# Kernel optimization log

Measured on AMD Instinct MI355X. Metric: run time of the kernel, lower is better.

The kernel has to match this reference:

```python
import jax, jax.numpy as jnp
import numpy as np


def setup_inputs() -> dict:
    key = jax.random.key(0)
    k1, k2, k3 = jax.random.split(key, 3)
    B, C, K, W, H = 8, 512, 512, 64, 64
    x = jax.random.normal(k1, (B, C, W, H), dtype=jnp.float32)
    y = jax.random.normal(k2, (B, K, W, H), dtype=jnp.float32)
    scale = jax.random.uniform(k3, (1,), dtype=jnp.float32)
    return {"x": x, "y": y, "scale": scale}


def reference(x, y, scale):
    B, C, W, H = x.shape
    K = y.shape[1]
    xq = x.reshape(B, C, W * H)            # [B, C, N]
    yk = y.reshape(B, K, W * H)            # [B, K, N]
    # energy = Q @ K^T : [B, C, K]
    energy = jnp.einsum('bcn,bkn->bck', xq, yk)
    # inverted max-subtract softmax over last dim (K)
    energy_new = jnp.max(energy, axis=-1, keepdims=True) - energy
    attention = jax.nn.softmax(energy_new, axis=-1)  # [B, C, K]
    # out = attention @ V : [B, C, N]
    out = jnp.einsum('bck,bkn->bcn', attention, yk).reshape(B, C, W, H)
    return x + scale * out
```

## Files before the change

kernel.cpp:

```cpp
#include <hip/hip_runtime.h>
#include <hip/hip_bf16.h>
#include <stdint.h>

#define BB 8
#define CC 512
#define KK 512
#define NN 4096

typedef __bf16 bf16x8 __attribute__((ext_vector_type(8)));
typedef float f32x4 __attribute__((ext_vector_type(4)));
typedef __attribute__((address_space(3))) uint8_t* lds_ptr_t;
typedef const __attribute__((address_space(1))) uint8_t* gbl_ptr_t;

static __device__ __forceinline__ unsigned short bf16_bits(float f) {
    __bf16 h = (__bf16)f;
    return __builtin_bit_cast(unsigned short, h);
}

__global__ void __launch_bounds__(256) split_hi_lo(const float* __restrict__ in,
        unsigned short* __restrict__ hi, unsigned short* __restrict__ lo, int n4) {
    int idx = blockIdx.x * blockDim.x + threadIdx.x;
    int stride = gridDim.x * blockDim.x;
    const float4* in4 = (const float4*)in;
    ushort4* h4 = (ushort4*)hi;
    ushort4* l4 = (ushort4*)lo;
    for (int i = idx; i < n4; i += stride) {
        float4 v = in4[i];
        float a[4] = {v.x, v.y, v.z, v.w};
        unsigned short hb[4], lb[4];
        #pragma unroll
        for (int j = 0; j < 4; ++j) {
            __bf16 h = (__bf16)a[j];
            float hf = (float)h;
            __bf16 l = (__bf16)(a[j] - hf);
            hb[j] = __builtin_bit_cast(unsigned short, h);
            lb[j] = __builtin_bit_cast(unsigned short, l);
        }
        h4[i] = make_ushort4(hb[0], hb[1], hb[2], hb[3]);
        l4[i] = make_ushort4(lb[0], lb[1], lb[2], lb[3]);
    }
}

__global__ void __launch_bounds__(256) energy_gemm(
        const unsigned short* __restrict__ xh, const unsigned short* __restrict__ xl,
        const unsigned short* __restrict__ yh, const unsigned short* __restrict__ yl,
        float* __restrict__ epart) {
    __shared__ __align__(16) uint8_t smem[4 * 16384];
    const int ktile = blockIdx.x;
    const int ctile = blockIdx.y;
    const int b = blockIdx.z >> 2;
    const int quarter = blockIdx.z & 3;
    const int t = threadIdx.x;
    const int wave = t >> 6, lane = t & 63;

    const size_t rowB = (size_t)NN * 2;
    const uint8_t* srcBase[4];
    srcBase[0] = (const uint8_t*)xh + ((size_t)b * CC + ctile * 128) * rowB + (size_t)quarter * 2048;
    srcBase[1] = (const uint8_t*)xl + ((size_t)b * CC + ctile * 128) * rowB + (size_t)quarter * 2048;
    srcBase[2] = (const uint8_t*)yh + ((size_t)b * KK + ktile * 128) * rowB + (size_t)quarter * 2048;
    srcBase[3] = (const uint8_t*)yl + ((size_t)b * KK + ktile * 128) * rowB + (size_t)quarter * 2048;

    f32x4 acc[4][4] = {};
    const int waveRow = wave >> 1, waveCol = wave & 1;

    for (int step = 0; step < 16; ++step) {
        const size_t colByte = (size_t)step * 128;
        #pragma unroll
        for (int i = 0; i < 16; ++i) {
            const int tile = i >> 2;
            const int lc = (i & 3) * 4 + wave;
            const int u = lc * 64 + lane;
            const int r = u >> 3;
            const int c3 = (u & 7) ^ (r & 7);
            const uint8_t* src = srcBase[tile] + (size_t)r * rowB + colByte + c3 * 16;
            __builtin_amdgcn_global_load_lds((gbl_ptr_t)src,
                (lds_ptr_t)(smem + tile * 16384 + lc * 1024), 16, 0, 0);
        }
        __syncthreads();
        #pragma unroll
        for (int kf = 0; kf < 2; ++kf) {
            bf16x8 fah[4], fal[4], fbh[4], fbl[4];
            #pragma unroll
            for (int m = 0; m < 4; ++m) {
                int r = waveRow * 64 + m * 16 + (lane & 15);
                int c3 = (kf * 4 + (lane >> 4)) ^ (r & 7);
                fah[m] = *(const bf16x8*)(smem + 0 * 16384 + r * 128 + c3 * 16);
                fal[m] = *(const bf16x8*)(smem + 1 * 16384 + r * 128 + c3 * 16);
            }
            #pragma unroll
            for (int n = 0; n < 4; ++n) {
                int r = waveCol * 64 + n * 16 + (lane & 15);
                int c3 = (kf * 4 + (lane >> 4)) ^ (r & 7);
                fbh[n] = *(const bf16x8*)(smem + 2 * 16384 + r * 128 + c3 * 16);
                fbl[n] = *(const bf16x8*)(smem + 3 * 16384 + r * 128 + c3 * 16);
            }
            #pragma unroll
            for (int m = 0; m < 4; ++m)
            #pragma unroll
            for (int n = 0; n < 4; ++n) {
                acc[m][n] = __builtin_amdgcn_mfma_f32_16x16x32_bf16(fah[m], fbh[n], acc[m][n], 0, 0, 0);
                acc[m][n] = __builtin_amdgcn_mfma_f32_16x16x32_bf16(fah[m], fbl[n], acc[m][n], 0, 0, 0);
                acc[m][n] = __builtin_amdgcn_mfma_f32_16x16x32_bf16(fal[m], fbh[n], acc[m][n], 0, 0, 0);
            }
        }
        __syncthreads();
    }

    float* eout = epart + (size_t)quarter * BB * CC * KK + (size_t)b * CC * KK;
    const int row0 = ctile * 128 + waveRow * 64;
    const int col0 = ktile * 128 + waveCol * 64;
    #pragma unroll
    for (int m = 0; m < 4; ++m)
    #pragma unroll
    for (int n = 0; n < 4; ++n)
    #pragma unroll
    for (int j = 0; j < 4; ++j) {
        int rr = row0 + m * 16 + (lane >> 4) * 4 + j;
        int cc2 = col0 + n * 16 + (lane & 15);
        eout[(size_t)rr * KK + cc2] = acc[m][n][j];
    }
}

__global__ void __launch_bounds__(256) softmax_inv(
        const float* __restrict__ e, unsigned short* __restrict__ att) {
    const int t = threadIdx.x;
    const int wave = t >> 6, lane = t & 63;
    const int row = blockIdx.x * 4 + wave;
    const size_t Q = (size_t)BB * CC * KK;
    const float* p0 = e + (size_t)row * KK;
    float v[8];
    float mn = 3.0e38f;
    #pragma unroll
    for (int i = 0; i < 8; ++i) {
        int c = lane + i * 64;
        v[i] = p0[c] + p0[Q + c] + p0[2 * Q + c] + p0[3 * Q + c];
        mn = fminf(mn, v[i]);
    }
    #pragma unroll
    for (int off = 32; off > 0; off >>= 1) mn = fminf(mn, __shfl_xor(mn, off));
    float p[8]; float s = 0.f;
    #pragma unroll
    for (int i = 0; i < 8; ++i) { p[i] = __expf(mn - v[i]); s += p[i]; }
    #pragma unroll
    for (int off = 32; off > 0; off >>= 1) s += __shfl_xor(s, off);
    float inv = 1.0f / s;
    unsigned short* arow = att + (size_t)row * KK;
    #pragma unroll
    for (int i = 0; i < 8; ++i) arow[lane + i * 64] = bf16_bits(p[i] * inv);
}

__global__ void __launch_bounds__(256) transpose_bf16(
        const unsigned short* __restrict__ yh, unsigned short* __restrict__ yT) {
    __shared__ unsigned short tile[64][66];
    const int n0 = blockIdx.x * 64, k0 = blockIdx.y * 64, b = blockIdx.z;
    const int t = threadIdx.x;
    const unsigned short* src = yh + (size_t)b * KK * NN;
    unsigned short* dst = yT + (size_t)b * NN * KK;
    #pragma unroll
    for (int i = 0; i < 2; ++i) {
        int idx = t + 256 * i;
        int r = idx >> 3;
        int c8 = (idx & 7) * 8;
        uint4 v = *(const uint4*)(src + (size_t)(k0 + r) * NN + n0 + c8);
        unsigned int w[4] = {v.x, v.y, v.z, v.w};
        #pragma unroll
        for (int q = 0; q < 4; ++q) {
            tile[r][c8 + 2 * q]     = (unsigned short)(w[q] & 0xffffu);
            tile[r][c8 + 2 * q + 1] = (unsigned short)(w[q] >> 16);
        }
    }
    __syncthreads();
    #pragma unroll
    for (int i = 0; i < 16; ++i) {
        int idx = t + 256 * i;
        int rn = idx >> 6;
        int ck = idx & 63;
        dst[(size_t)(n0 + rn) * KK + k0 + ck] = tile[ck][rn];
    }
}

__global__ void __launch_bounds__(256) pv_residual(
        const unsigned short* __restrict__ att, const unsigned short* __restrict__ yT,
        const float* __restrict__ x, const float* __restrict__ scale,
        float* __restrict__ out) {
    __shared__ __align__(16) uint8_t smem[2 * 16384];
    const int ntile = blockIdx.x;
    const int ctile = blockIdx.y;
    const int b = blockIdx.z;
    const int t = threadIdx.x;
    const int wave = t >> 6, lane = t & 63;
    const size_t rowB = (size_t)KK * 2;
    const uint8_t* srcA = (const uint8_t*)att + ((size_t)b * CC + ctile * 128) * rowB;
    const uint8_t* srcB = (const uint8_t*)yT  + ((size_t)b * NN + ntile * 128) * rowB;

    f32x4 acc[4][4] = {};
    const int waveRow = wave >> 1, waveCol = wave & 1;

    for (int step = 0; step < 8; ++step) {
        const size_t colByte = (size_t)step * 128;
        #pragma unroll
        for (int i = 0; i < 8; ++i) {
            const uint8_t* base = (i < 4) ? srcA : srcB;
            const int tile = i >> 2;
            const int lc = (i & 3) * 4 + wave;
            const int u = lc * 64 + lane;
            const int r = u >> 3;
            const int c3 = (u & 7) ^ (r & 7);
            const uint8_t* src = base + (size_t)r * rowB + colByte + c3 * 16;
            __builtin_amdgcn_global_load_lds((gbl_ptr_t)src,
                (lds_ptr_t)(smem + tile * 16384 + lc * 1024), 16, 0, 0);
        }
        __syncthreads();
        #pragma unroll
        for (int kf = 0; kf < 2; ++kf) {
            bf16x8 fa[4], fb[4];
            #pragma unroll
            for (int m = 0; m < 4; ++m) {
                int r = waveRow * 64 + m * 16 + (lane & 15);
                int c3 = (kf * 4 + (lane >> 4)) ^ (r & 7);
                fa[m] = *(const bf16x8*)(smem + r * 128 + c3 * 16);
            }
            #pragma unroll
            for (int n = 0; n < 4; ++n) {
                int r = waveCol * 64 + n * 16 + (lane & 15);
                int c3 = (kf * 4 + (lane >> 4)) ^ (r & 7);
                fb[n] = *(const bf16x8*)(smem + 16384 + r * 128 + c3 * 16);
            }
            #pragma unroll
            for (int m = 0; m < 4; ++m)
            #pragma unroll
            for (int n = 0; n < 4; ++n)
                acc[m][n] = __builtin_amdgcn_mfma_f32_16x16x32_bf16(fa[m], fb[n], acc[m][n], 0, 0, 0);
        }
        __syncthreads();
    }

    const float s = scale[0];
    const int row0 = ctile * 128 + waveRow * 64;
    const int col0 = ntile * 128 + waveCol * 64;
    #pragma unroll
    for (int m = 0; m < 4; ++m)
    #pragma unroll
    for (int n = 0; n < 4; ++n)
    #pragma unroll
    for (int j = 0; j < 4; ++j) {
        int rr = row0 + m * 16 + (lane >> 4) * 4 + j;
        int cc2 = col0 + n * 16 + (lane & 15);
        size_t idx = ((size_t)b * CC + rr) * NN + cc2;
        out[idx] = x[idx] + s * acc[m][n][j];
    }
}

extern "C" void kernel_launch(void* const* d_in, const int* in_sizes, int n_in,
                              void* d_out, int out_size, void* d_ws, size_t ws_size,
                              hipStream_t stream) {
    const float* x = (const float*)d_in[0];
    const float* y = (const float*)d_in[1];
    const float* scale = (const float*)d_in[2];
    float* out = (float*)d_out;
    uint8_t* ws = (uint8_t*)d_ws;
    const size_t MB = 1024 * 1024;
    unsigned short* xh = (unsigned short*)(ws + 0 * MB);
    unsigned short* xl = (unsigned short*)(ws + 32 * MB);
    unsigned short* yh = (unsigned short*)(ws + 64 * MB);
    unsigned short* yl = (unsigned short*)(ws + 96 * MB);
    float* epart = out;
    unsigned short* yT  = (unsigned short*)(ws + 0 * MB);
    unsigned short* att = (unsigned short*)(ws + 32 * MB);

    const int n4 = BB * CC * NN / 4;
    split_hi_lo<<<4096, 256, 0, stream>>>(x, xh, xl, n4);
    split_hi_lo<<<4096, 256, 0, stream>>>(y, yh, yl, n4);
    energy_gemm<<<dim3(4, 4, BB * 4), 256, 0, stream>>>(xh, xl, yh, yl, epart);
    transpose_bf16<<<dim3(NN / 64, KK / 64, BB), 256, 0, stream>>>(yh, yT);
    softmax_inv<<<dim3(BB * CC / 4), 256, 0, stream>>>(epart, att);
    pv_residual<<<dim3(NN / 128, CC / 128, BB), 256, 0, stream>>>(att, yT, x, scale, out);
}
```

Baseline: 302.3 us.

## Fuse y split with transpose and remap GEMM blocks for XCD locality

Replaces the separate y hi/lo split and bf16 transpose kernels with one kernel. It splits y into hi/lo and writes the transposed hi copy from an LDS tile, so the extra pass that re-reads yh and one launch go away. The energy and PV GEMMs move to a 1D grid with index remapping, so blocks sharing a batch or slice land on the same XCD and can share its L2. Workspace buffers are rearranged, with xl and the energy partials now placed in the output buffer.

```diff
diff --git a/kernel.cpp b/kernel.cpp
--- a/kernel.cpp
+++ b/kernel.cpp
@@ -41,15 +41,61 @@
     }
 }
 
+__global__ void __launch_bounds__(256) split_y_T(const float* __restrict__ y,
+        unsigned short* __restrict__ yh, unsigned short* __restrict__ yl,
+        unsigned short* __restrict__ yT) {
+    __shared__ unsigned short tile[64][66];
+    const int n0 = blockIdx.x * 64, k0 = blockIdx.y * 64, b = blockIdx.z;
+    const int t = threadIdx.x;
+    const float* src = y + (size_t)b * KK * NN;
+    unsigned short* dsth = yh + (size_t)b * KK * NN;
+    unsigned short* dstl = yl + (size_t)b * KK * NN;
+    unsigned short* dstT = yT + (size_t)b * NN * KK;
+    #pragma unroll
+    for (int i = 0; i < 4; ++i) {
+        int idx = t + 256 * i;
+        int r = idx >> 4;
+        int c4 = (idx & 15) * 4;
+        float4 v = *(const float4*)(src + (size_t)(k0 + r) * NN + n0 + c4);
+        float a[4] = {v.x, v.y, v.z, v.w};
+        unsigned short hb[4], lb[4];
+        #pragma unroll
+        for (int q = 0; q < 4; ++q) {
+            __bf16 h = (__bf16)a[q];
+            float hf = (float)h;
+            __bf16 l = (__bf16)(a[q] - hf);
+            hb[q] = __builtin_bit_cast(unsigned short, h);
+            lb[q] = __builtin_bit_cast(unsigned short, l);
+            tile[r][c4 + q] = hb[q];
+        }
+        size_t off = (size_t)(k0 + r) * NN + n0 + c4;
+        *(ushort4*)(dsth + off) = make_ushort4(hb[0], hb[1], hb[2], hb[3]);
+        *(ushort4*)(dstl + off) = make_ushort4(lb[0], lb[1], lb[2], lb[3]);
+    }
+    __syncthreads();
+    #pragma unroll
+    for (int i = 0; i < 16; ++i) {
+        int idx = t + 256 * i;
+        int rn = idx >> 6;
+        int ck = idx & 63;
+        dstT[(size_t)(n0 + rn) * KK + k0 + ck] = tile[ck][rn];
+    }
+}
+
 __global__ void __launch_bounds__(256) energy_gemm(
         const unsigned short* __restrict__ xh, const unsigned short* __restrict__ xl,
         const unsigned short* __restrict__ yh, const unsigned short* __restrict__ yl,
         float* __restrict__ epart) {
     __shared__ __align__(16) uint8_t smem[4 * 16384];
-    const int ktile = blockIdx.x;
-    const int ctile = blockIdx.y;
-    const int b = blockIdx.z >> 2;
-    const int quarter = blockIdx.z & 3;
+    const int j = blockIdx.x;
+    const int xcd = j & 7;
+    const int rem = j >> 3;
+    const int ktile = rem & 3;
+    const int ctile = (rem >> 2) & 3;
+    const int sgrp = rem >> 4;
+    const int slice = xcd + 8 * sgrp;
+    const int b = slice >> 2;
+    const int quarter = slice & 3;
     const int t = threadIdx.x;
     const int wave = t >> 6, lane = t & 63;
 
@@ -114,10 +160,10 @@
     #pragma unroll
     for (int n = 0; n < 4; ++n)
     #pragma unroll
-    for (int j = 0; j < 4; ++j) {
-        int rr = row0 + m * 16 + (lane >> 4) * 4 + j;
+    for (int jj = 0; jj < 4; ++jj) {
+        int rr = row0 + m * 16 + (lane >> 4) * 4 + jj;
         int cc2 = col0 + n * 16 + (lane & 15);
-        eout[(size_t)rr * KK + cc2] = acc[m][n][j];
+        eout[(size_t)rr * KK + cc2] = acc[m][n][jj];
     }
 }
 
@@ -149,44 +195,16 @@
     for (int i = 0; i < 8; ++i) arow[lane + i * 64] = bf16_bits(p[i] * inv);
 }
 
-__global__ void __launch_bounds__(256) transpose_bf16(
-        const unsigned short* __restrict__ yh, unsigned short* __restrict__ yT) {
-    __shared__ unsigned short tile[64][66];
-    const int n0 = blockIdx.x * 64, k0 = blockIdx.y * 64, b = blockIdx.z;
-    const int t = threadIdx.x;
-    const unsigned short* src = yh + (size_t)b * KK * NN;
-    unsigned short* dst = yT + (size_t)b * NN * KK;
-    #pragma unroll
-    for (int i = 0; i < 2; ++i) {
-        int idx = t + 256 * i;
-        int r = idx >> 3;
-        int c8 = (idx & 7) * 8;
-        uint4 v = *(const uint4*)(src + (size_t)(k0 + r) * NN + n0 + c8);
-        unsigned int w[4] = {v.x, v.y, v.z, v.w};
-        #pragma unroll
-        for (int q = 0; q < 4; ++q) {
-            tile[r][c8 + 2 * q]     = (unsigned short)(w[q] & 0xffffu);
-            tile[r][c8 + 2 * q + 1] = (unsigned short)(w[q] >> 16);
-        }
-    }
-    __syncthreads();
-    #pragma unroll
-    for (int i = 0; i < 16; ++i) {
-        int idx = t + 256 * i;
-        int rn = idx >> 6;
-        int ck = idx & 63;
-        dst[(size_t)(n0 + rn) * KK + k0 + ck] = tile[ck][rn];
-    }
-}
-
 __global__ void __launch_bounds__(256) pv_residual(
         const unsigned short* __restrict__ att, const unsigned short* __restrict__ yT,
         const float* __restrict__ x, const float* __restrict__ scale,
         float* __restrict__ out) {
     __shared__ __align__(16) uint8_t smem[2 * 16384];
-    const int ntile = blockIdx.x;
-    const int ctile = blockIdx.y;
-    const int b = blockIdx.z;
+    const int j = blockIdx.x;
+    const int b = j & 7;
+    const int rem2 = j >> 3;
+    const int ntile = rem2 & 31;
+    const int ctile = rem2 >> 5;
     const int t = threadIdx.x;
     const int wave = t >> 6, lane = t & 63;
     const size_t rowB = (size_t)KK * 2;
@@ -243,11 +261,11 @@
     #pragma unroll
     for (int n = 0; n < 4; ++n)
     #pragma unroll
-    for (int j = 0; j < 4; ++j) {
-        int rr = row0 + m * 16 + (lane >> 4) * 4 + j;
+    for (int jj = 0; jj < 4; ++jj) {
+        int rr = row0 + m * 16 + (lane >> 4) * 4 + jj;
         int cc2 = col0 + n * 16 + (lane & 15);
         size_t idx = ((size_t)b * CC + rr) * NN + cc2;
-        out[idx] = x[idx] + s * acc[m][n][j];
+        out[idx] = x[idx] + s * acc[m][n][jj];
     }
 }
 
@@ -259,20 +277,20 @@
     const float* scale = (const float*)d_in[2];
     float* out = (float*)d_out;
     uint8_t* ws = (uint8_t*)d_ws;
+    uint8_t* ob = (uint8_t*)d_out;
     const size_t MB = 1024 * 1024;
     unsigned short* xh = (unsigned short*)(ws + 0 * MB);
-    unsigned short* xl = (unsigned short*)(ws + 32 * MB);
-    unsigned short* yh = (unsigned short*)(ws + 64 * MB);
-    unsigned short* yl = (unsigned short*)(ws + 96 * MB);
-    float* epart = out;
-    unsigned short* yT  = (unsigned short*)(ws + 0 * MB);
-    unsigned short* att = (unsigned short*)(ws + 32 * MB);
+    unsigned short* yh = (unsigned short*)(ws + 32 * MB);
+    unsigned short* yl = (unsigned short*)(ws + 64 * MB);
+    unsigned short* yT = (unsigned short*)(ws + 96 * MB);
+    unsigned short* att = (unsigned short*)(ws + 128 * MB);
+    float* epart = (float*)(ob + 0 * MB);
+    unsigned short* xl = (unsigned short*)(ob + 32 * MB);
 
     const int n4 = BB * CC * NN / 4;
     split_hi_lo<<<4096, 256, 0, stream>>>(x, xh, xl, n4);
-    split_hi_lo<<<4096, 256, 0, stream>>>(y, yh, yl, n4);
-    energy_gemm<<<dim3(4, 4, BB * 4), 256, 0, stream>>>(xh, xl, yh, yl, epart);
-    transpose_bf16<<<dim3(NN / 64, KK / 64, BB), 256, 0, stream>>>(yh, yT);
-    softmax_inv<<<dim3(BB * CC / 4), 256, 0, stream>>>(epart, att);
-    pv_residual<<<dim3(NN / 128, CC / 128, BB), 256, 0, stream>>>(att, yT, x, scale, out);
-}
+    split_y_T<<<dim3(NN / 64, KK / 64, BB), 256, 0, stream>>>(y, yh, yl, yT);
+    energy_gemm<<<512, 256, 0, stream>>>(xh, xl, yh, yl, epart);
+    softmax_inv<<<BB * CC / 4, 256, 0, stream>>>(epart, att);
+    pv_residual<<<1024, 256, 0, stream>>>(att, yT, x, scale, out);
+}
```

Measured after the change: 294.1 us. -2.7%, faster.
